# Kernel optimization log

Hardware: AMD Instinct MI355X
Metric: run time of the kernel (lower is better)

The kernel has to match this reference:

```python
import jax, jax.numpy as jnp
import numpy as np
import math

NTOKEN, NINP, NHID, SEQ, BATCH = 33278, 400, 1150, 70, 16
ODE_STEPS = 8  # fixed-step RK4 over t in [0,1] (reference for the adaptive solver)


def lstm_layer(x, h0, c0, Wih, Whh, bih, bhh):
    # x: [S, B, in]; PyTorch gate order i, f, g, o
    def step(carry, xt):
        h, c = carry
        g = xt @ Wih.T + h @ Whh.T + bih + bhh
        i, f, gg, o = jnp.split(g, 4, axis=-1)
        c = jax.nn.sigmoid(f) * c + jax.nn.sigmoid(i) * jnp.tanh(gg)
        h = jax.nn.sigmoid(o) * jnp.tanh(c)
        return (h, c), h
    (hT, cT), ys = jax.lax.scan(step, (h0, c0), x)
    return ys, hT, cT


def cnf_delta_logp(E, cnf_W, cnf_b):
    # ODEnet: f(t,z) = relu(Linear(concat([t, z]))); exact divergence since
    # Jacobian diag = relu'(pre) * diag(Wx). Integrates dz/dt=f, d(dlogp)/dt=-div f.
    wt = cnf_W[:, 0]
    Wx = cnf_W[:, 1:]
    dWx = jnp.diag(Wx)

    def f(t, z):
        pre = z @ Wx.T + t * wt + cnf_b          # [ntoken, ninp]
        div = jnp.sum((pre > 0) * dWx, axis=-1)  # exact trace of df/dz
        return jax.nn.relu(pre), -div

    dt = 1.0 / ODE_STEPS

    def rk4(carry, t):
        z, dl = carry
        k1z, k1l = f(t, z)
        k2z, k2l = f(t + dt / 2, z + dt / 2 * k1z)
        k3z, k3l = f(t + dt / 2, z + dt / 2 * k2z)
        k4z, k4l = f(t + dt, z + dt * k3z)
        z = z + dt / 6 * (k1z + 2 * k2z + 2 * k3z + k4z)
        dl = dl + dt / 6 * (k1l + 2 * k2l + 2 * k3l + k4l)
        return (z, dl), None

    ts = jnp.arange(ODE_STEPS, dtype=E.dtype) * dt
    (zT, dl), _ = jax.lax.scan(rk4, (E, jnp.zeros(E.shape[0], E.dtype)), ts)
    return dl  # [ntoken]


def setup_inputs() -> dict:
    key = jax.random.key(0)
    ks = jax.random.split(key, 16)
    s = 0.1
    inp = {
        "tokens": jax.random.randint(ks[0], (SEQ, BATCH), 0, NTOKEN),
        "h0_0": jnp.zeros((BATCH, NHID), jnp.float32),
        "c0_0": jnp.zeros((BATCH, NHID), jnp.float32),
        "h0_1": jnp.zeros((BATCH, NHID), jnp.float32),
        "c0_1": jnp.zeros((BATCH, NHID), jnp.float32),
        "h0_2": jnp.zeros((BATCH, NINP), jnp.float32),
        "c0_2": jnp.zeros((BATCH, NINP), jnp.float32),
        "emb_W": jax.random.uniform(ks[1], (NTOKEN, NINP), jnp.float32, -s, s),
        "Wih0": jax.random.normal(ks[2], (4 * NHID, NINP), jnp.float32) * 0.02,
        "Whh0": jax.random.normal(ks[3], (4 * NHID, NHID), jnp.float32) * 0.02,
        "bih0": jnp.zeros((4 * NHID,), jnp.float32),
        "bhh0": jnp.zeros((4 * NHID,), jnp.float32),
        "Wih1": jax.random.normal(ks[4], (4 * NHID, NHID), jnp.float32) * 0.02,
        "Whh1": jax.random.normal(ks[5], (4 * NHID, NHID), jnp.float32) * 0.02,
        "bih1": jnp.zeros((4 * NHID,), jnp.float32),
        "bhh1": jnp.zeros((4 * NHID,), jnp.float32),
        "Wih2": jax.random.normal(ks[6], (4 * NINP, NHID), jnp.float32) * 0.02,
        "Whh2": jax.random.normal(ks[7], (4 * NINP, NINP), jnp.float32) * 0.02,
        "bih2": jnp.zeros((4 * NINP,), jnp.float32),
        "bhh2": jnp.zeros((4 * NINP,), jnp.float32),
        "cnf_W": jax.random.normal(ks[8], (NINP, NINP + 1), jnp.float32) * 0.05,
        "cnf_b": jnp.zeros((NINP,), jnp.float32),
    }
    return inp


def reference(tokens, h0_0, c0_0, h0_1, c0_1, h0_2, c0_2, emb_W,
              Wih0, Whh0, bih0, bhh0, Wih1, Whh1, bih1, bhh1,
              Wih2, Whh2, bih2, bhh2, cnf_W, cnf_b):
    # embedding (eval mode: all dropouts are identity)
    x = emb_W[tokens]                               # [S, B, ninp]
    x, h1, c1 = lstm_layer(x, h0_0, c0_0, Wih0, Whh0, bih0, bhh0)
    x, h2, c2 = lstm_layer(x, h0_1, c0_1, Wih1, Whh1, bih1, bhh1)
    x, h3, c3 = lstm_layer(x, h0_2, c0_2, Wih2, Whh2, bih2, bhh2)
    # nhidlast == ninp -> no latent projection
    h = x.reshape(SEQ * BATCH, NINP)

    # MVNLogProb vectorized: -0.5 ||E_v - h_i||^2 - k/2 log(2*pi)
    e2 = jnp.sum(emb_W * emb_W, axis=-1)            # [ntoken]
    h2n = jnp.sum(h * h, axis=-1, keepdims=True)    # [SB, 1]
    sq = e2[None, :] - 2.0 * (h @ emb_W.T) + h2n    # [SB, ntoken]
    log_pz0 = -0.5 * sq - (NINP / 2.0) * math.log(2.0 * math.pi)

    # CNF delta_logp is identical for every token position (loop-invariant)
    delta = cnf_delta_logp(emb_W, cnf_W, cnf_b)     # [ntoken]
    log_pz1 = log_pz0 - delta[None, :]

    prob = jax.nn.softmax(log_pz1, axis=-1)
    log_prob = jnp.log(prob + 1e-8)
    model_output = log_prob.reshape(SEQ, BATCH, NTOKEN)
    return model_output, h1, c1, h2, c2, h3, c3
```

## Files before the change

### kernel.cpp

```cpp
#include <hip/hip_runtime.h>
#include <hip/hip_bf16.h>
#include <math.h>

#define SEQL 70
#define NTOK 33278
#define ODE_STEPS 8
#define NBLK 242
#define CZ4 404

typedef __attribute__((ext_vector_type(4))) float f32x4;
typedef __attribute__((ext_vector_type(8))) short s16x8;
typedef unsigned short u16;

__device__ __forceinline__ u16 f2b(float f) {
    union { float f; unsigned int u; } a; a.f = f;
    unsigned int u = a.u;
    return (u16)((u + 0x7FFFu + ((u >> 16) & 1u)) >> 16);
}
__device__ __forceinline__ float b2f(u16 s) {
    union { unsigned int u; float f; } a; a.u = ((unsigned int)s) << 16;
    return a.f;
}

__device__ __forceinline__ unsigned czoff(int row, int colb) {
    unsigned s = ((colb < 768 ? (row & 7) : (row & 3)) << 4);
    return (unsigned)(row * 832 + (colb ^ (int)s));
}

__global__ void cvt_pad_k(const float* __restrict__ src, u16* __restrict__ dst,
                          int G, int Nin, int Nop, int Kin, int Kp, int rs, int co) {
    size_t total = (size_t)G * Nop * Kp;
    for (size_t idx = (size_t)blockIdx.x * 256 + threadIdx.x; idx < total;
         idx += (size_t)gridDim.x * 256) {
        int k = (int)(idx % Kp);
        size_t t2 = idx / Kp;
        int j = (int)(t2 % Nop);
        int g = (int)(t2 / Nop);
        float v = 0.f;
        if (j < Nin && k < Kin) v = src[((size_t)g * Nin + j) * rs + co + k];
        dst[idx] = f2b(v);
    }
}

__global__ void bias_k(const float* __restrict__ bih, const float* __restrict__ bhh,
                       float* __restrict__ o, int Nin, int Nop) {
    int idx = blockIdx.x * 256 + threadIdx.x;
    if (idx >= 4 * Nop) return;
    int g = idx / Nop, j = idx % Nop;
    o[idx] = (j < Nin) ? (bih[g * Nin + j] + bhh[g * Nin + j]) : 0.f;
}

__global__ void wtdwx_k(const float* __restrict__ cw, float* __restrict__ wt,
                        float* __restrict__ dwx) {
    int i = blockIdx.x * 256 + threadIdx.x;
    if (i < 400) {
        wt[i]  = cw[(size_t)i * 401];
        dwx[i] = cw[(size_t)i * 401 + 1 + i];
    }
}

__global__ void h0cvt_k(const float* __restrict__ h0, u16* __restrict__ hb, int N, int Kp) {
    int idx = blockIdx.x * 256 + threadIdx.x;
    if (idx >= 16 * Kp) return;
    int b = idx / Kp, k = idx % Kp;
    hb[idx] = f2b(k < N ? h0[b * N + k] : 0.f);
}

__global__ void embed_k(const int* __restrict__ tok, const float* __restrict__ emb,
                        u16* __restrict__ x0) {
    int idx = blockIdx.x * 256 + threadIdx.x;
    if (idx >= 1152 * 416) return;
    int r = idx / 416, k = idx - r * 416;
    float v = 0.f;
    if (r < SEQL * 16 && k < 400) v = emb[(size_t)tok[r] * 400 + k];
    x0[idx] = f2b(v);
}

__global__ void rowsumsq_k(const float* __restrict__ X, float* __restrict__ o, int K) {
    int r = blockIdx.x;
    const float* xr = X + (size_t)r * K;
    int lane = threadIdx.x;
    float s = 0.f;
    for (int k = lane; k < K; k += 64) { float v = xr[k]; s += v * v; }
#pragma unroll
    for (int off = 1; off < 64; off <<= 1) s += __shfl_xor(s, off, 64);
    if (lane == 0) o[r] = s;
}

__global__ void ucomb_k(const float* __restrict__ e2, const float* __restrict__ dl,
                        float* __restrict__ u) {
    int i = blockIdx.x * 256 + threadIdx.x;
    if (i < NTOK) u[i] = -0.5f * e2[i] - dl[i];
}

__global__ void gemm_bt_k(const u16* __restrict__ A, const u16* __restrict__ B,
                          float* __restrict__ C, int Kp, int lda, int ldb, int ldc,
                          int Mreal, int Nreal, const float* __restrict__ uvec) {
    const int tid = threadIdx.x;
    const int wid = tid >> 6, lane = tid & 63;
    const int la = lane & 15, lk = (lane >> 4) * 8;
    const int m0 = blockIdx.y * 64 + wid * 16;
    const int n0 = blockIdx.x * 64;
    const f32x4 Z4 = {0.f, 0.f, 0.f, 0.f};
    f32x4 acc[4] = {Z4, Z4, Z4, Z4};
    const u16* Ar = A + (size_t)(m0 + la) * lda + lk;
    const u16* Br = B + (size_t)(n0 + la) * ldb + lk;
    for (int k = 0; k < Kp; k += 32) {
        s16x8 a = *(const s16x8*)(Ar + k);
#pragma unroll
        for (int nt = 0; nt < 4; ++nt) {
            s16x8 b = *(const s16x8*)(Br + (size_t)nt * 16 * ldb + k);
            acc[nt] = __builtin_amdgcn_mfma_f32_16x16x32_bf16(a, b, acc[nt], 0, 0, 0);
        }
    }
    const int mr = m0 + (lane >> 4) * 4;
#pragma unroll
    for (int nt = 0; nt < 4; ++nt) {
        int cc = n0 + nt * 16 + la;
        if (cc >= Nreal) continue;
        float uv = uvec ? uvec[cc] : 0.f;
#pragma unroll
        for (int r = 0; r < 4; ++r) {
            int rr = mr + r;
            if (rr < Mreal) C[(size_t)rr * ldc + cc] = acc[nt][r] + uv;
        }
    }
}

__device__ __forceinline__ void flatbar(int* cnt, int* gen, int nb, int iter) {
    __syncthreads();
    if (threadIdx.x == 0) {
        int old = __hip_atomic_fetch_add(cnt, 1, __ATOMIC_ACQ_REL, __HIP_MEMORY_SCOPE_AGENT);
        if ((old % nb) == nb - 1)
            __hip_atomic_fetch_add(gen, 1, __ATOMIC_ACQ_REL, __HIP_MEMORY_SCOPE_AGENT);
        while (__hip_atomic_load(gen, __ATOMIC_RELAXED, __HIP_MEMORY_SCOPE_AGENT) <= iter)
            __builtin_amdgcn_s_sleep(2);
        (void)__hip_atomic_load(gen, __ATOMIC_ACQUIRE, __HIP_MEMORY_SCOPE_AGENT);
    }
    __syncthreads();
}
__device__ __forceinline__ void waitgen(int* gen, int needed) {
    if (threadIdx.x == 0) {
        while (__hip_atomic_load(gen, __ATOMIC_RELAXED, __HIP_MEMORY_SCOPE_AGENT) < needed)
            __builtin_amdgcn_s_sleep(2);
        (void)__hip_atomic_load(gen, __ATOMIC_ACQUIRE, __HIP_MEMORY_SCOPE_AGENT);
    }
    __syncthreads();
}

__global__ __launch_bounds__(768, 3) void lstm_k(
    const float* __restrict__ c00, const float* __restrict__ c01,
    const float* __restrict__ c02,
    const u16* __restrict__ Whh0p, const u16* __restrict__ Wih1p,
    const u16* __restrict__ Whh1p, const u16* __restrict__ Wih2p,
    const u16* __restrict__ Whh2p,
    const float* __restrict__ xW0, const float* __restrict__ bias2v,
    const float* __restrict__ bias1v,
    u16* __restrict__ ys0s, u16* __restrict__ ys1s, u16* __restrict__ ys2s,
    float* __restrict__ oh1, float* __restrict__ oc1,
    float* __restrict__ oh2, float* __restrict__ oc2,
    float* __restrict__ oh3, float* __restrict__ oc3,
    int* __restrict__ bar)
{
    __shared__ __align__(16) char smem[162816];
    u16* wlds = (u16*)smem;
    float* gl = (float*)(smem + 147456);
    const int tid = threadIdx.x;
    const int bid = blockIdx.x;
    const int wv = tid >> 6, lane = tid & 63;
    const int la = lane & 15, lg = lane >> 4;

    int role, jb;
    if (bid < 72) { role = 0; jb = bid; }
    else if (bid < 216) { role = 1; jb = bid - 72; }
    else { role = 2; jb = bid - 216; }

    int* c0 = bar;        int* g0 = bar + 16;
    int* c1 = bar + 32;   int* g1 = bar + 48;
    int* c2 = bar + 64;   int* g2 = bar + 80;

    if (role == 0) {
        for (int s = tid; s < 4 * 36 * 64; s += 768) {
            int ln = s & 63, kt = (s >> 6) % 36, nt = s / (36 * 64);
            int row = nt * 1152 + jb * 16 + (ln & 15);
            int col = kt * 32 + (ln >> 4) * 8;
            *(s16x8*)(wlds + (size_t)s * 8) =
                *(const s16x8*)(Whh0p + (size_t)row * 1152 + col);
        }
    } else if (role == 1) {
        for (int s = tid; s < 2 * 72 * 64; s += 768) {
            int ln = s & 63, kt = (s >> 6) % 72, nt = s / (72 * 64);
            int lr = nt * 16 + (ln & 15);
            int row = (lr >> 3) * 1152 + jb * 8 + (lr & 7);
            int col8 = (ln >> 4) * 8;
            const u16* src = (kt < 36)
                ? Wih1p + (size_t)row * 1152 + kt * 32 + col8
                : Whh1p + (size_t)row * 1152 + (kt - 36) * 32 + col8;
            *(s16x8*)(wlds + (size_t)s * 8) = *(const s16x8*)src;
        }
    }
    __syncthreads();

    float c_reg = 0.f;
    for (int t = 0; t < SEQL; ++t) {
        if (role == 1) waitgen(g0, t + 1);
        else if (role == 2) waitgen(g1, t + 1);

        f32x4 acc = {0.f, 0.f, 0.f, 0.f};
        if (role == 0) {
            int nt = wv / 3, kg = wv - nt * 3;
            const u16* ar = ys0s + ((size_t)t * 16 + la) * 1152 + lg * 8;
            for (int kt = kg * 12; kt < kg * 12 + 12; ++kt) {
                s16x8 a = *(const s16x8*)(ar + kt * 32);
                s16x8 b = *(const s16x8*)(wlds + ((size_t)(nt * 36 + kt) * 64 + lane) * 8);
                acc = __builtin_amdgcn_mfma_f32_16x16x32_bf16(a, b, acc, 0, 0, 0);
            }
            *(f32x4*)(gl + wv * 320 + la * 20 + lg * 4) = acc;
        } else if (role == 1) {
            int nt = wv / 6, kg = wv - nt * 6;
            const u16* ax = ys0s + ((size_t)(t + 1) * 16 + la) * 1152 + lg * 8;
            const u16* ah = ys1s + ((size_t)t * 16 + la) * 1152 + lg * 8;
            for (int kt = kg * 12; kt < kg * 12 + 12; ++kt) {
                s16x8 a = (kt < 36) ? *(const s16x8*)(ax + kt * 32)
                                    : *(const s16x8*)(ah + (kt - 36) * 32);
                s16x8 b = *(const s16x8*)(wlds + ((size_t)(nt * 72 + kt) * 64 + lane) * 8);
                acc = __builtin_amdgcn_mfma_f32_16x16x32_bf16(a, b, acc, 0, 0, 0);
            }
            *(f32x4*)(gl + wv * 320 + la * 20 + lg * 4) = acc;
        } else {
            int nt = wv / 3, kg = wv - nt * 3;
            int k0 = (kg * 49) / 3, k1 = ((kg + 1) * 49) / 3;
            const u16* ax = ys1s + ((size_t)(t + 1) * 16 + la) * 1152 + lg * 8;
            const u16* ah = ys2s + ((size_t)t * 16 + la) * 416 + lg * 8;
            int wr = nt * 416 + jb * 16 + la;
            for (int kt = k0; kt < k1; ++kt) {
                s16x8 a, b;
                if (kt < 36) {
                    a = *(const s16x8*)(ax + kt * 32);
                    b = *(const s16x8*)(Wih2p + (size_t)wr * 1152 + kt * 32 + lg * 8);
                } else {
                    a = *(const s16x8*)(ah + (kt - 36) * 32);
                    b = *(const s16x8*)(Whh2p + (size_t)wr * 416 + (kt - 36) * 32 + lg * 8);
                }
                acc = __builtin_amdgcn_mfma_f32_16x16x32_bf16(a, b, acc, 0, 0, 0);
            }
            *(f32x4*)(gl + wv * 320 + la * 20 + lg * 4) = acc;
        }
        __syncthreads();
        if (role == 1) {
            if (tid < 128) {
                int u = tid & 7, tb = tid >> 3;
                int ug = jb * 8 + u;
                float gv[4];
#pragma unroll
                for (int g = 0; g < 4; ++g) {
                    int lr = g * 8 + u;
                    int nt = lr >> 4, li = lr & 15;
                    float s = 0.f;
#pragma unroll
                    for (int kg = 0; kg < 6; ++kg)
                        s += gl[(nt * 6 + kg) * 320 + li * 20 + tb];
                    gv[g] = s + bias1v[g * 1152 + ug];
                }
                float cprev = (t == 0) ? ((ug < 1150) ? c01[tb * 1150 + ug] : 0.f) : c_reg;
                float si = 1.f / (1.f + expf(-gv[0]));
                float sf = 1.f / (1.f + expf(-gv[1]));
                float so = 1.f / (1.f + expf(-gv[3]));
                float cn = sf * cprev + si * tanhf(gv[2]);
                float hn = so * tanhf(cn);
                c_reg = cn;
                if (ug < 1150) {
                    ys1s[((size_t)(t + 1) * 16 + tb) * 1152 + ug] = f2b(hn);
                    if (t == SEQL - 1) { oh2[tb * 1150 + ug] = hn; oc2[tb * 1150 + ug] = cn; }
                }
            }
        } else if (tid < 256) {
            int u = tid & 15, tb = tid >> 4;
            int ug = jb * 16 + u;
            float gv[4];
#pragma unroll
            for (int g = 0; g < 4; ++g) {
                float s = 0.f;
#pragma unroll
                for (int kg = 0; kg < 3; ++kg)
                    s += gl[(g * 3 + kg) * 320 + u * 20 + tb];
                gv[g] = s + ((role == 0)
                             ? xW0[((size_t)t * 16 + tb) * 4608 + g * 1152 + ug]
                             : bias2v[g * 416 + ug]);
            }
            int N = (role == 0) ? 1150 : 400;
            const float* c0i = (role == 0) ? c00 : c02;
            float cprev = (t == 0) ? ((ug < N) ? c0i[tb * N + ug] : 0.f) : c_reg;
            float si = 1.f / (1.f + expf(-gv[0]));
            float sf = 1.f / (1.f + expf(-gv[1]));
            float so = 1.f / (1.f + expf(-gv[3]));
            float cn = sf * cprev + si * tanhf(gv[2]);
            float hn = so * tanhf(cn);
            c_reg = cn;
            if (ug < N) {
                if (role == 0) {
                    ys0s[((size_t)(t + 1) * 16 + tb) * 1152 + ug] = f2b(hn);
                    if (t == SEQL - 1) { oh1[tb * 1150 + ug] = hn; oc1[tb * 1150 + ug] = cn; }
                } else {
                    ys2s[((size_t)(t + 1) * 16 + tb) * 416 + ug] = f2b(hn);
                    if (t == SEQL - 1) { oh3[tb * 400 + ug] = hn; oc3[tb * 400 + ug] = cn; }
                }
            }
        }
        if (role == 0) flatbar(c0, g0, 72, t);
        else if (role == 1) flatbar(c1, g1, 144, t);
        else flatbar(c2, g2, 26, t);
    }
}

__global__ __launch_bounds__(512, 1) void cnf_k(const float* __restrict__ emb,
                                                const u16* __restrict__ Wxp,
                                                const float* __restrict__ wtv,
                                                const float* __restrict__ bvv,
                                                const float* __restrict__ dwxv,
                                                float* __restrict__ dl) {
    __shared__ __align__(16) char smem[158720];
    float* z0s = (float*)smem;
    char*  zib = smem + 64 * CZ4 * 4;
    float* dsc = (float*)(smem + 64 * CZ4 * 4 + 64 * 832);
    const int tid = threadIdx.x;
    const int m0 = blockIdx.x * 64;
    const int wv = tid >> 6, lane = tid & 63;
    const int la = lane & 15, lg = lane >> 4;

    for (int idx = tid; idx < 64 * 416; idx += 512) {
        int r = idx / 416, cc = idx - r * 416;
        int row = m0 + r;
        float v = (cc < 400 && row < NTOK) ? emb[(size_t)row * 400 + cc] : 0.f;
        if (cc < 400) z0s[r * CZ4 + cc] = v;
        *(u16*)(zib + czoff(r, cc * 2)) = f2b(v);
    }

    const int tb0 = (wv * 25) >> 3;
    const int Qw = (((wv + 1) * 25) >> 3) - tb0;
    const f32x4 Z4 = {0.f, 0.f, 0.f, 0.f};
    f32x4 wt4[4], bv4[4], dw4[4];
#pragma unroll
    for (int q = 0; q < 4; ++q) {
        wt4[q] = Z4; bv4[q] = Z4; dw4[q] = Z4;
        if (q < Qw) {
            int c4 = (tb0 + q) * 16 + lg * 4;
            wt4[q] = *(const f32x4*)(wtv + c4);
            bv4[q] = *(const f32x4*)(bvv + c4);
            dw4[q] = *(const f32x4*)(dwxv + c4);
        }
    }
    __syncthreads();

    const float dt = 1.f / ODE_STEPS, dt6 = dt / 6.f;
    f32x4 Aacc[4][4];
#pragma unroll
    for (int m = 0; m < 4; ++m)
#pragma unroll
        for (int q = 0; q < 4; ++q) Aacc[m][q] = Z4;
    float divacc[4] = {0.f, 0.f, 0.f, 0.f};

#pragma unroll 1
    for (int st = 0; st < ODE_STEPS; ++st) {
        float t0 = st * dt;
#pragma unroll 1
        for (int s = 0; s < 4; ++s) {
            float ts = t0 + ((s == 0) ? 0.f : (s == 3) ? dt : 0.5f * dt);
            float wgt = (s == 1 || s == 2) ? 2.f : 1.f;
            float cs = (s == 2) ? dt : 0.5f * dt;
            f32x4 pre[4][4];
#pragma unroll
            for (int m = 0; m < 4; ++m)
#pragma unroll
                for (int q = 0; q < 4; ++q) pre[m][q] = Z4;
#pragma unroll 1
            for (int kk = 0; kk < 13; ++kk) {
                s16x8 aW[4];
#pragma unroll
                for (int q = 0; q < 4; ++q)
                    if (q < Qw)
                        aW[q] = *(const s16x8*)(Wxp + (size_t)((tb0 + q) * 16 + la) * 416 +
                                                kk * 32 + lg * 8);
#pragma unroll
                for (int m = 0; m < 4; ++m) {
                    int rr = m * 16 + la;
                    s16x8 bz = *(const s16x8*)(zib + czoff(rr, (kk * 32 + lg * 8) * 2));
#pragma unroll
                    for (int q = 0; q < 4; ++q)
                        if (q < Qw)
                            pre[m][q] = __builtin_amdgcn_mfma_f32_16x16x32_bf16(
                                aW[q], bz, pre[m][q], 0, 0, 0);
                }
            }
            __syncthreads();
            f32x4 tb4[4], dwg[4];
#pragma unroll
            for (int q = 0; q < 4; ++q)
                if (q < Qw) { tb4[q] = ts * wt4[q] + bv4[q]; dwg[q] = wgt * dw4[q]; }
#pragma unroll
            for (int m = 0; m < 4; ++m) {
                int row = m * 16 + la;
#pragma unroll
                for (int q = 0; q < 4; ++q) {
                    if (q >= Qw) continue;
                    int c4 = (tb0 + q) * 16 + lg * 4;
                    f32x4 z04 = *(const f32x4*)(z0s + row * CZ4 + c4);
                    f32x4 ev;
#pragma unroll
                    for (int r = 0; r < 4; ++r) {
                        float pv = pre[m][q][r] + tb4[q][r];
                        float kz = fmaxf(pv, 0.f);
                        if (pv > 0.f) divacc[m] += dwg[q][r];
                        if (s < 3) {
                            Aacc[m][q][r] += wgt * kz;
                            ev[r] = z04[r] + cs * kz;
                        } else {
                            float zn = z04[r] + dt6 * (Aacc[m][q][r] + kz);
                            ev[r] = zn; z04[r] = zn; Aacc[m][q][r] = 0.f;
                        }
                    }
                    if (s == 3) *(f32x4*)(z0s + row * CZ4 + c4) = z04;
                    ushort4 pk;
                    pk.x = f2b(ev[0]); pk.y = f2b(ev[1]);
                    pk.z = f2b(ev[2]); pk.w = f2b(ev[3]);
                    *(ushort4*)(zib + czoff(row, c4 * 2)) = pk;
                }
            }
            __syncthreads();
        }
    }
#pragma unroll
    for (int m = 0; m < 4; ++m) {
        float v = divacc[m];
        v += __shfl_xor(v, 16, 64);
        v += __shfl_xor(v, 32, 64);
        if (lane < 16) dsc[wv * 64 + m * 16 + la] = v;
    }
    __syncthreads();
    for (int row = tid; row < 64; row += 512) {
        float s = 0.f;
#pragma unroll
        for (int w = 0; w < 8; ++w) s += dsc[w * 64 + row];
        if (m0 + row < NTOK) dl[m0 + row] = -dt6 * s;
    }
}

__global__ void logsoftmax_k(float* __restrict__ L, int n) {
    const int row = blockIdx.x;
    float* R = L + (size_t)row * n;
    const int tid = threadIdx.x;
    float mx = -INFINITY, s = 0.f;
    for (int c = tid; c < n; c += 256) {
        float v = R[c];
        float nm = fmaxf(mx, v);
        s = s * expf(mx - nm) + expf(v - nm);
        mx = nm;
    }
#pragma unroll
    for (int off = 1; off < 64; off <<= 1) {
        float om = __shfl_xor(mx, off, 64);
        float os = __shfl_xor(s, off, 64);
        float nm = fmaxf(mx, om);
        s = s * expf(mx - nm) + os * expf(om - nm);
        mx = nm;
    }
    __shared__ float smx[4], ssm[4];
    if ((tid & 63) == 0) { smx[tid >> 6] = mx; ssm[tid >> 6] = s; }
    __syncthreads();
    float bm = fmaxf(fmaxf(smx[0], smx[1]), fmaxf(smx[2], smx[3]));
    float bs = ssm[0] * expf(smx[0] - bm) + ssm[1] * expf(smx[1] - bm) +
               ssm[2] * expf(smx[2] - bm) + ssm[3] * expf(smx[3] - bm);
    float lz = logf(bs);
    for (int c = tid; c < n; c += 256) {
        float v = R[c];
        R[c] = logf(expf(v - bm) + 1e-8f * bs) - lz;
    }
}

extern "C" void kernel_launch(void* const* d_in, const int* in_sizes, int n_in,
                              void* d_out, int out_size, void* d_ws, size_t ws_size,
                              hipStream_t stream) {
    const int*   tokens = (const int*)d_in[0];
    const float* h00 = (const float*)d_in[1];
    const float* c00 = (const float*)d_in[2];
    const float* h01 = (const float*)d_in[3];
    const float* c01 = (const float*)d_in[4];
    const float* h02 = (const float*)d_in[5];
    const float* c02 = (const float*)d_in[6];
    const float* embW = (const float*)d_in[7];
    const float* Wih0 = (const float*)d_in[8];
    const float* Whh0 = (const float*)d_in[9];
    const float* bih0 = (const float*)d_in[10];
    const float* bhh0 = (const float*)d_in[11];
    const float* Wih1 = (const float*)d_in[12];
    const float* Whh1 = (const float*)d_in[13];
    const float* bih1 = (const float*)d_in[14];
    const float* bhh1 = (const float*)d_in[15];
    const float* Wih2 = (const float*)d_in[16];
    const float* Whh2 = (const float*)d_in[17];
    const float* bih2 = (const float*)d_in[18];
    const float* bhh2 = (const float*)d_in[19];
    const float* cnfW = (const float*)d_in[20];
    const float* cnfb = (const float*)d_in[21];
    float* out = (float*)d_out;

    char* p = (char*)d_ws;
    auto alloc = [&](size_t bytes) -> void* {
        void* r = (void*)p;
        p += (bytes + 255) & ~(size_t)255;
        return r;
    };
    u16*   emb_p = (u16*)alloc((size_t)33280 * 416 * 2);
    u16*   x0    = (u16*)alloc((size_t)1152 * 416 * 2);
    u16*   ys0s  = (u16*)alloc((size_t)1136 * 1152 * 2);
    u16*   ys1s  = (u16*)alloc((size_t)1136 * 1152 * 2);
    u16*   ys2s  = (u16*)alloc((size_t)1184 * 416 * 2);
    float* xW    = (float*)alloc((size_t)1120 * 4608 * 4);
    u16*   Wih0p = (u16*)alloc((size_t)4608 * 416 * 2);
    u16*   Whh0p = (u16*)alloc((size_t)4608 * 1152 * 2);
    u16*   Wih1p = (u16*)alloc((size_t)4608 * 1152 * 2);
    u16*   Whh1p = (u16*)alloc((size_t)4608 * 1152 * 2);
    u16*   Wih2p = (u16*)alloc((size_t)1664 * 1152 * 2);
    u16*   Whh2p = (u16*)alloc((size_t)1664 * 416 * 2);
    float* bias0 = (float*)alloc((size_t)4608 * 4);
    float* bias1 = (float*)alloc((size_t)4608 * 4);
    float* bias2 = (float*)alloc((size_t)1664 * 4);
    u16*   Wxp   = (u16*)alloc((size_t)416 * 416 * 2);
    float* wtv   = (float*)alloc((size_t)400 * 4);
    float* dwx   = (float*)alloc((size_t)400 * 4);
    float* dl    = (float*)alloc((size_t)NTOK * 4);
    float* e2    = (float*)alloc((size_t)NTOK * 4);
    float* uvec  = (float*)alloc((size_t)NTOK * 4);
    int*   bar   = (int*)alloc(4096);

    size_t OM = (size_t)SEQL * 16 * NTOK;
    float* oh1 = out + OM;
    float* oc1 = oh1 + 16 * 1150;
    float* oh2 = oc1 + 16 * 1150;
    float* oc2 = oh2 + 16 * 1150;
    float* oh3 = oc2 + 16 * 1150;
    float* oc3 = oh3 + 16 * 400;

    hipMemsetAsync(bar, 0, 4096, stream);
    hipMemsetAsync(ys0s, 0, (size_t)1136 * 1152 * 2, stream);
    hipMemsetAsync(ys1s, 0, (size_t)1136 * 1152 * 2, stream);
    hipMemsetAsync(ys2s, 0, (size_t)1184 * 416 * 2, stream);

    cvt_pad_k<<<2048, 256, 0, stream>>>(Wih0, Wih0p, 4, 1150, 1152, 400, 416, 400, 0);
    cvt_pad_k<<<2048, 256, 0, stream>>>(Whh0, Whh0p, 4, 1150, 1152, 1150, 1152, 1150, 0);
    cvt_pad_k<<<2048, 256, 0, stream>>>(Wih1, Wih1p, 4, 1150, 1152, 1150, 1152, 1150, 0);
    cvt_pad_k<<<2048, 256, 0, stream>>>(Whh1, Whh1p, 4, 1150, 1152, 1150, 1152, 1150, 0);
    cvt_pad_k<<<2048, 256, 0, stream>>>(Wih2, Wih2p, 4, 400, 416, 1150, 1152, 1150, 0);
    cvt_pad_k<<<2048, 256, 0, stream>>>(Whh2, Whh2p, 4, 400, 416, 400, 416, 400, 0);
    cvt_pad_k<<<2048, 256, 0, stream>>>(embW, emb_p, 1, 33278, 33280, 400, 416, 400, 0);
    cvt_pad_k<<<2048, 256, 0, stream>>>(cnfW, Wxp, 1, 400, 416, 400, 416, 401, 1);
    bias_k<<<(4 * 1152 + 255) / 256, 256, 0, stream>>>(bih0, bhh0, bias0, 1150, 1152);
    bias_k<<<(4 * 1152 + 255) / 256, 256, 0, stream>>>(bih1, bhh1, bias1, 1150, 1152);
    bias_k<<<(4 * 416 + 255) / 256, 256, 0, stream>>>(bih2, bhh2, bias2, 400, 416);
    wtdwx_k<<<2, 256, 0, stream>>>(cnfW, wtv, dwx);
    rowsumsq_k<<<NTOK, 64, 0, stream>>>(embW, e2, 400);

    h0cvt_k<<<(16 * 1152 + 255) / 256, 256, 0, stream>>>(h00, ys0s, 1150, 1152);
    h0cvt_k<<<(16 * 1152 + 255) / 256, 256, 0, stream>>>(h01, ys1s, 1150, 1152);
    h0cvt_k<<<(16 * 416 + 255) / 256, 256, 0, stream>>>(h02, ys2s, 400, 416);

    cnf_k<<<520, 512, 0, stream>>>(embW, Wxp, wtv, cnfb, dwx, dl);
    ucomb_k<<<(NTOK + 255) / 256, 256, 0, stream>>>(e2, dl, uvec);

    embed_k<<<(1152 * 416 + 255) / 256, 256, 0, stream>>>(tokens, embW, x0);
    gemm_bt_k<<<dim3(72, 18), 256, 0, stream>>>(x0, Wih0p, xW, 416, 416, 416, 4608,
                                                1120, 4608, bias0);

    lstm_k<<<NBLK, 768, 0, stream>>>(
        c00, c01, c02, Whh0p, Wih1p, Whh1p, Wih2p, Whh2p,
        xW, bias2, bias1, ys0s, ys1s, ys2s,
        oh1, oc1, oh2, oc2, oh3, oc3, bar);

    gemm_bt_k<<<dim3(520, 18), 256, 0, stream>>>(ys2s + (size_t)16 * 416, emb_p, out,
                                                 416, 416, 416, NTOK, 1120, NTOK, uvec);
    logsoftmax_k<<<1120, 256, 0, stream>>>(out, NTOK);
}
```

Measured before the change: 3.016 ms.

## Double-buffer CNF stage state in LDS, keep z0 in registers, enlarge output GEMM tile

The CNF kernel no longer keeps the fp32 z0 state in shared memory. It holds it in registers, and the bf16 stage input is double-buffered so each RK stage needs one barrier instead of two. The smaller LDS footprint and launch_bounds(512,2) aim to fit two blocks per CU. The output GEMM gets a 128-row tile variant that reuses each B fragment across two A rows, halving the number of B loads. Extra register pressure from the z0 arrays could cause spills under the tighter launch bound.

```diff
diff --git a/kernel.cpp b/kernel.cpp
--- a/kernel.cpp
+++ b/kernel.cpp
@@ -6,7 +6,7 @@
 #define NTOK 33278
 #define ODE_STEPS 8
 #define NBLK 242
-#define CZ4 404
+#define ZH 53248
 
 typedef __attribute__((ext_vector_type(4))) float f32x4;
 typedef __attribute__((ext_vector_type(8))) short s16x8;
@@ -123,6 +123,50 @@
         for (int r = 0; r < 4; ++r) {
             int rr = mr + r;
             if (rr < Mreal) C[(size_t)rr * ldc + cc] = acc[nt][r] + uv;
+        }
+    }
+}
+
+__global__ void gemm_bt128_k(const u16* __restrict__ A, const u16* __restrict__ B,
+                             float* __restrict__ C, int Kp, int lda, int ldb, int ldc,
+                             int Mreal, int Nreal, const float* __restrict__ uvec) {
+    const int tid = threadIdx.x;
+    const int wid = tid >> 6, lane = tid & 63;
+    const int la = lane & 15, lk = (lane >> 4) * 8;
+    const int m0 = blockIdx.y * 128 + wid * 16;
+    const int n0 = blockIdx.x * 64;
+    const f32x4 Z4 = {0.f, 0.f, 0.f, 0.f};
+    f32x4 acc[2][4];
+#pragma unroll
+    for (int h = 0; h < 2; ++h)
+#pragma unroll
+        for (int nt = 0; nt < 4; ++nt) acc[h][nt] = Z4;
+    const u16* Ar0 = A + (size_t)(m0 + la) * lda + lk;
+    const u16* Ar1 = Ar0 + (size_t)64 * lda;
+    const u16* Br = B + (size_t)(n0 + la) * ldb + lk;
+    for (int k = 0; k < Kp; k += 32) {
+        s16x8 a0 = *(const s16x8*)(Ar0 + k);
+        s16x8 a1 = *(const s16x8*)(Ar1 + k);
+#pragma unroll
+        for (int nt = 0; nt < 4; ++nt) {
+            s16x8 b = *(const s16x8*)(Br + (size_t)nt * 16 * ldb + k);
+            acc[0][nt] = __builtin_amdgcn_mfma_f32_16x16x32_bf16(a0, b, acc[0][nt], 0, 0, 0);
+            acc[1][nt] = __builtin_amdgcn_mfma_f32_16x16x32_bf16(a1, b, acc[1][nt], 0, 0, 0);
+        }
+    }
+#pragma unroll
+    for (int h = 0; h < 2; ++h) {
+        const int mr = m0 + h * 64 + (lane >> 4) * 4;
+#pragma unroll
+        for (int nt = 0; nt < 4; ++nt) {
+            int cc = n0 + nt * 16 + la;
+            if (cc >= Nreal) continue;
+            float uv = uvec ? uvec[cc] : 0.f;
+#pragma unroll
+            for (int r = 0; r < 4; ++r) {
+                int rr = mr + r;
+                if (rr < Mreal) C[(size_t)rr * ldc + cc] = acc[h][nt][r] + uv;
+            }
         }
     }
 }
@@ -313,16 +357,18 @@
     }
 }
 
-__global__ __launch_bounds__(512, 1) void cnf_k(const float* __restrict__ emb,
+__global__ __launch_bounds__(512, 2) void cnf_k(const float* __restrict__ emb,
                                                 const u16* __restrict__ Wxp,
                                                 const float* __restrict__ wtv,
                                                 const float* __restrict__ bvv,
                                                 const float* __restrict__ dwxv,
                                                 float* __restrict__ dl) {
-    __shared__ __align__(16) char smem[158720];
-    float* z0s = (float*)smem;
-    char*  zib = smem + 64 * CZ4 * 4;
-    float* dsc = (float*)(smem + 64 * CZ4 * 4 + 64 * 832);
+    __shared__ __align__(16) char smem[113536];
+    char*  zib = smem;
+    float* dsc = (float*)(smem + 2 * ZH);
+    float* wtL = (float*)(smem + 2 * ZH + 2048);
+    float* bvL = (float*)(smem + 2 * ZH + 2048 + 1664);
+    float* dwL = (float*)(smem + 2 * ZH + 2048 + 3328);
     const int tid = threadIdx.x;
     const int m0 = blockIdx.x * 64;
     const int wv = tid >> 6, lane = tid & 63;
@@ -332,22 +378,27 @@
         int r = idx / 416, cc = idx - r * 416;
         int row = m0 + r;
         float v = (cc < 400 && row < NTOK) ? emb[(size_t)row * 400 + cc] : 0.f;
-        if (cc < 400) z0s[r * CZ4 + cc] = v;
         *(u16*)(zib + czoff(r, cc * 2)) = f2b(v);
+    }
+    for (int i = tid; i < 400; i += 512) {
+        wtL[i] = wtv[i]; bvL[i] = bvv[i]; dwL[i] = dwxv[i];
     }
 
     const int tb0 = (wv * 25) >> 3;
     const int Qw = (((wv + 1) * 25) >> 3) - tb0;
     const f32x4 Z4 = {0.f, 0.f, 0.f, 0.f};
-    f32x4 wt4[4], bv4[4], dw4[4];
-#pragma unroll
-    for (int q = 0; q < 4; ++q) {
-        wt4[q] = Z4; bv4[q] = Z4; dw4[q] = Z4;
-        if (q < Qw) {
-            int c4 = (tb0 + q) * 16 + lg * 4;
-            wt4[q] = *(const f32x4*)(wtv + c4);
-            bv4[q] = *(const f32x4*)(bvv + c4);
-            dw4[q] = *(const f32x4*)(dwxv + c4);
+
+    f32x4 z0r[4][4];
+#pragma unroll
+    for (int m = 0; m < 4; ++m) {
+        int row = m0 + m * 16 + la;
+#pragma unroll
+        for (int q = 0; q < 4; ++q) {
+            z0r[m][q] = Z4;
+            if (q < Qw && row < NTOK) {
+                int c4 = (tb0 + q) * 16 + lg * 4;
+                z0r[m][q] = *(const f32x4*)(emb + (size_t)row * 400 + c4);
+            }
         }
     }
     __syncthreads();
@@ -361,73 +412,75 @@
     float divacc[4] = {0.f, 0.f, 0.f, 0.f};
 
 #pragma unroll 1
-    for (int st = 0; st < ODE_STEPS; ++st) {
-        float t0 = st * dt;
+    for (int stg = 0; stg < 4 * ODE_STEPS; ++stg) {
+        const int st = stg >> 2, s = stg & 3;
+        const float t0 = st * dt;
+        const float ts = t0 + ((s == 0) ? 0.f : (s == 3) ? dt : 0.5f * dt);
+        const float wgt = (s == 1 || s == 2) ? 2.f : 1.f;
+        const float cs = (s == 2) ? dt : 0.5f * dt;
+        char* cur = zib + (size_t)(stg & 1) * ZH;
+        char* nxt = zib + (size_t)((stg + 1) & 1) * ZH;
+
+        f32x4 pre[4][4];
+#pragma unroll
+        for (int m = 0; m < 4; ++m)
+#pragma unroll
+            for (int q = 0; q < 4; ++q) pre[m][q] = Z4;
 #pragma unroll 1
-        for (int s = 0; s < 4; ++s) {
-            float ts = t0 + ((s == 0) ? 0.f : (s == 3) ? dt : 0.5f * dt);
-            float wgt = (s == 1 || s == 2) ? 2.f : 1.f;
-            float cs = (s == 2) ? dt : 0.5f * dt;
-            f32x4 pre[4][4];
-#pragma unroll
-            for (int m = 0; m < 4; ++m)
-#pragma unroll
-                for (int q = 0; q < 4; ++q) pre[m][q] = Z4;
-#pragma unroll 1
-            for (int kk = 0; kk < 13; ++kk) {
-                s16x8 aW[4];
+        for (int kk = 0; kk < 13; ++kk) {
+            s16x8 aW[4];
+#pragma unroll
+            for (int q = 0; q < 4; ++q)
+                if (q < Qw)
+                    aW[q] = *(const s16x8*)(Wxp + (size_t)((tb0 + q) * 16 + la) * 416 +
+                                            kk * 32 + lg * 8);
+#pragma unroll
+            for (int m = 0; m < 4; ++m) {
+                int rr = m * 16 + la;
+                s16x8 bz = *(const s16x8*)(cur + czoff(rr, (kk * 32 + lg * 8) * 2));
 #pragma unroll
                 for (int q = 0; q < 4; ++q)
                     if (q < Qw)
-                        aW[q] = *(const s16x8*)(Wxp + (size_t)((tb0 + q) * 16 + la) * 416 +
-                                                kk * 32 + lg * 8);
-#pragma unroll
-                for (int m = 0; m < 4; ++m) {
-                    int rr = m * 16 + la;
-                    s16x8 bz = *(const s16x8*)(zib + czoff(rr, (kk * 32 + lg * 8) * 2));
-#pragma unroll
-                    for (int q = 0; q < 4; ++q)
-                        if (q < Qw)
-                            pre[m][q] = __builtin_amdgcn_mfma_f32_16x16x32_bf16(
-                                aW[q], bz, pre[m][q], 0, 0, 0);
+                        pre[m][q] = __builtin_amdgcn_mfma_f32_16x16x32_bf16(
+                            aW[q], bz, pre[m][q], 0, 0, 0);
+            }
+        }
+        f32x4 tb4[4], dwg[4];
+#pragma unroll
+        for (int q = 0; q < 4; ++q)
+            if (q < Qw) {
+                int c4 = (tb0 + q) * 16 + lg * 4;
+                tb4[q] = ts * (*(const f32x4*)(wtL + c4)) + *(const f32x4*)(bvL + c4);
+                dwg[q] = wgt * (*(const f32x4*)(dwL + c4));
+            }
+#pragma unroll
+        for (int m = 0; m < 4; ++m) {
+            int row = m * 16 + la;
+#pragma unroll
+            for (int q = 0; q < 4; ++q) {
+                if (q >= Qw) continue;
+                int c4 = (tb0 + q) * 16 + lg * 4;
+                f32x4 ev;
+#pragma unroll
+                for (int r = 0; r < 4; ++r) {
+                    float pv = pre[m][q][r] + tb4[q][r];
+                    float kz = fmaxf(pv, 0.f);
+                    if (pv > 0.f) divacc[m] += dwg[q][r];
+                    if (s < 3) {
+                        Aacc[m][q][r] += wgt * kz;
+                        ev[r] = z0r[m][q][r] + cs * kz;
+                    } else {
+                        float zn = z0r[m][q][r] + dt6 * (Aacc[m][q][r] + kz);
+                        ev[r] = zn; z0r[m][q][r] = zn; Aacc[m][q][r] = 0.f;
+                    }
                 }
-            }
-            __syncthreads();
-            f32x4 tb4[4], dwg[4];
-#pragma unroll
-            for (int q = 0; q < 4; ++q)
-                if (q < Qw) { tb4[q] = ts * wt4[q] + bv4[q]; dwg[q] = wgt * dw4[q]; }
-#pragma unroll
-            for (int m = 0; m < 4; ++m) {
-                int row = m * 16 + la;
-#pragma unroll
-                for (int q = 0; q < 4; ++q) {
-                    if (q >= Qw) continue;
-                    int c4 = (tb0 + q) * 16 + lg * 4;
-                    f32x4 z04 = *(const f32x4*)(z0s + row * CZ4 + c4);
-                    f32x4 ev;
-#pragma unroll
-                    for (int r = 0; r < 4; ++r) {
-                        float pv = pre[m][q][r] + tb4[q][r];
-                        float kz = fmaxf(pv, 0.f);
-                        if (pv > 0.f) divacc[m] += dwg[q][r];
-                        if (s < 3) {
-                            Aacc[m][q][r] += wgt * kz;
-                            ev[r] = z04[r] + cs * kz;
-                        } else {
-                            float zn = z04[r] + dt6 * (Aacc[m][q][r] + kz);
-                            ev[r] = zn; z04[r] = zn; Aacc[m][q][r] = 0.f;
-                        }
-                    }
-                    if (s == 3) *(f32x4*)(z0s + row * CZ4 + c4) = z04;
-                    ushort4 pk;
-                    pk.x = f2b(ev[0]); pk.y = f2b(ev[1]);
-                    pk.z = f2b(ev[2]); pk.w = f2b(ev[3]);
-                    *(ushort4*)(zib + czoff(row, c4 * 2)) = pk;
-                }
-            }
-            __syncthreads();
-        }
+                ushort4 pk;
+                pk.x = f2b(ev[0]); pk.y = f2b(ev[1]);
+                pk.z = f2b(ev[2]); pk.w = f2b(ev[3]);
+                *(ushort4*)(nxt + czoff(row, c4 * 2)) = pk;
+            }
+        }
+        __syncthreads();
     }
 #pragma unroll
     for (int m = 0; m < 4; ++m) {
@@ -576,7 +629,7 @@
         xW, bias2, bias1, ys0s, ys1s, ys2s,
         oh1, oc1, oh2, oc2, oh3, oc3, bar);
 
-    gemm_bt_k<<<dim3(520, 18), 256, 0, stream>>>(ys2s + (size_t)16 * 416, emb_p, out,
-                                                 416, 416, 416, NTOK, 1120, NTOK, uvec);
+    gemm_bt128_k<<<dim3(520, 9), 256, 0, stream>>>(ys2s + (size_t)16 * 416, emb_p, out,
+                                                   416, 416, 416, NTOK, 1120, NTOK, uvec);
     logsoftmax_k<<<1120, 256, 0, stream>>>(out, NTOK);
 }
```

New measurement: 2.999 ms. No clear change (-0.6%).
